# Kernel optimization log

Measured on AMD Instinct MI355X. Metric: run time of the kernel, lower is better.

Reference implementation:

```python
import jax, jax.numpy as jnp
import numpy as np

FEATURE_DIM = 16
NUM_HEADS = 16
HEAD_DIM = 64
R2 = float(np.sqrt(2.0))
RD = float(np.sqrt(FEATURE_DIM))        # sqrt(d) = 4
RRD = float(np.sqrt(RD))                # d^(1/4) = 2
RMS_EPS = 1e-5


def taylor_exp(x):
    # x: [b, h, l, d] -> [b, h, l, 1 + d + d*d]
    x2 = (x[..., :, None] * x[..., None, :]).reshape(*x.shape[:-1], FEATURE_DIM * FEATURE_DIM) / R2
    ones = jnp.ones_like(x[..., :1])
    return jnp.concatenate([ones, x / RRD, x2 / RD], axis=-1)


def setup_inputs() -> dict:
    key = jax.random.key(0)
    ks = jax.random.split(key, 5)
    b, l, d_model = 4, 2048, 1024
    inp = {
        'hidden_states': jax.random.normal(ks[0], (b, l, d_model), dtype=jnp.float32),
        'Wq': jax.random.normal(ks[1], (FEATURE_DIM * NUM_HEADS, d_model), dtype=jnp.float32) * 0.02,
        'Wk': jax.random.normal(ks[2], (FEATURE_DIM * NUM_HEADS, d_model), dtype=jnp.float32) * 0.02,
        'Wv': jax.random.normal(ks[3], (NUM_HEADS * HEAD_DIM, d_model), dtype=jnp.float32) * 0.02,
        'Wo': jax.random.normal(ks[4], (d_model, NUM_HEADS * HEAD_DIM), dtype=jnp.float32) * 0.02,
        'g_weight': jnp.ones((HEAD_DIM,), dtype=jnp.float32),
    }
    return inp


def reference(hidden_states, Wq, Wk, Wv, Wo, g_weight):
    b, l, _ = hidden_states.shape
    # projections (Linear, no bias): x @ W.T
    q = (hidden_states @ Wq.T).reshape(b, l, NUM_HEADS, FEATURE_DIM).transpose(0, 2, 1, 3)
    k = (hidden_states @ Wk.T).reshape(b, l, NUM_HEADS, FEATURE_DIM).transpose(0, 2, 1, 3)
    v = (hidden_states @ Wv.T).reshape(b, l, NUM_HEADS, HEAD_DIM).transpose(0, 2, 1, 3)

    qf = taylor_exp(q)  # [b, h, l, 273]
    kf = taylor_exp(k)  # [b, h, l, 273]

    A_qk = jnp.einsum('bhnd,bhmd->bhnm', qf, kf)
    A_qk = jnp.tril(A_qk)
    y = jnp.einsum('bhnm,bhme->bhne', A_qk, v)  # [b, h, l, head_dim]

    kv_state = jnp.einsum('bhnd,bhnf->bhfd', kf, v)[:, :, None]  # [b, h, 1, head_dim, 273]

    # RMSNorm over head_dim
    rms = jax.lax.rsqrt(jnp.mean(y * y, axis=-1, keepdims=True) + RMS_EPS)
    y = y * rms * g_weight

    y = y.transpose(0, 2, 1, 3).reshape(b, l, NUM_HEADS * HEAD_DIM)
    out = y @ Wo.T
    return out, kv_state
```

## Files before the change

kernel.cpp:

```cpp
#include <hip/hip_runtime.h>


typedef unsigned short u16;
typedef unsigned int u32;
typedef __attribute__((ext_vector_type(4))) float f32x4;
typedef __attribute__((ext_vector_type(16))) float f32x16;
typedef __attribute__((ext_vector_type(8))) short s16x8;

struct MaskT { static constexpr bool value = true;  };
struct MaskF { static constexpr bool value = false; };

__device__ __forceinline__ float bf2f(u16 u) {
    union { unsigned int i; float f; } x; x.i = ((unsigned int)u) << 16; return x.f;
}
__device__ __forceinline__ u16 f2bf(float f) {
    union { float f; unsigned int u; } x; x.f = f;
    unsigned int r = x.u + 0x7FFFu + ((x.u >> 16) & 1u);
    return (u16)(r >> 16);
}

typedef const __attribute__((address_space(1))) u32* gas1_t;
typedef __attribute__((address_space(3))) u32* las3_t;
__device__ __forceinline__ void gld16(const u16* g, u16* l) {
    __builtin_amdgcn_global_load_lds((gas1_t)(const void*)g, (las3_t)(void*)l, 16, 0, 0);
}

__global__ void detect_kernel(const unsigned int* __restrict__ H, int* __restrict__ flag)
{
    const int lane = threadIdx.x;
    int cnt = 0;
#pragma unroll
    for (int i = 0; i < 16; ++i) {
        const unsigned int wrd = H[lane * 16 + i];
        const int e = (int)((wrd >> 7) & 0xFFu);
        if (e >= 85 && e <= 170) ++cnt;
    }
    cnt += __shfl_xor(cnt, 1);  cnt += __shfl_xor(cnt, 2);
    cnt += __shfl_xor(cnt, 4);  cnt += __shfl_xor(cnt, 8);
    cnt += __shfl_xor(cnt, 16); cnt += __shfl_xor(cnt, 32);
    if (lane == 0) *flag = (cnt < 700) ? 1 : 0;
}

__global__ __launch_bounds__(256)
void cvt_all_kernel(const void* __restrict__ H,  const void* __restrict__ Wq,
                    const void* __restrict__ Wk, const void* __restrict__ Wv,
                    const void* __restrict__ Wo, const void* __restrict__ gw,
                    u16* __restrict__ Hb,  u16* __restrict__ Wqb,
                    u16* __restrict__ Wkb, u16* __restrict__ Wvb,
                    u16* __restrict__ Wob, u16* __restrict__ gwb,
                    const int* __restrict__ flag)
{
    const int f32in = *flag;
    const int NQ = 11010112 / 4;
    for (int qi = blockIdx.x * 256 + threadIdx.x; qi < NQ; qi += gridDim.x * 256) {
        const int i = qi * 4;
        const void* src; u16* dst; int off;
        if      (i <  8388608) { src = H;  dst = Hb;  off = i; }
        else if (i <  8650752) { src = Wq; dst = Wqb; off = i - 8388608; }
        else if (i <  8912896) { src = Wk; dst = Wkb; off = i - 8650752; }
        else if (i <  9961472) { src = Wv; dst = Wvb; off = i - 8912896; }
        else if (i < 11010048) { src = Wo; dst = Wob; off = i - 9961472; }
        else                   { src = gw; dst = gwb; off = i - 11010048; }
        ushort4 o;
        if (f32in) {
            const float4 v = *((const float4*)src + (off >> 2));
            o.x = f2bf(v.x); o.y = f2bf(v.y); o.z = f2bf(v.z); o.w = f2bf(v.w);
        } else {
            o = *((const ushort4*)src + (off >> 2));
        }
        *(ushort4*)(dst + off) = o;
    }
}

template<int MODE>
__global__ __launch_bounds__(256)
void gemm_nt(const u16* __restrict__ A,
             const u16* __restrict__ Bq, const u16* __restrict__ Bk,
             const u16* __restrict__ Bv,
             u16* __restrict__ Oq, u16* __restrict__ Ok,
             u16* __restrict__ Ovt, float* __restrict__ Of)
{
    __shared__ __attribute__((aligned(16))) u16 As[8192];
    __shared__ __attribute__((aligned(16))) u16 Bs[8192];
    const int t = threadIdx.x;
    const int lane = t & 63, w = t >> 6;
    const int c = lane & 15, qd = lane >> 4;
    const int wm = (w >> 1) * 64, wn = (w & 1) * 64;
    const int nwgx = gridDim.x;
    const int pid = blockIdx.y * nwgx + blockIdx.x;
    const int lid = (pid & 7) * ((nwgx * 64) >> 3) + (pid >> 3);
    const int rm = (lid / nwgx) * 128;
    const int cb = (lid % nwgx) * 128;

    const u16* Bsrc; int wrow0;
    if (MODE == 0) {
        if (cb < 256)      { Bsrc = Bq; wrow0 = cb; }
        else if (cb < 512) { Bsrc = Bk; wrow0 = cb - 256; }
        else               { Bsrc = Bv; wrow0 = cb - 512; }
    } else { Bsrc = Bq; wrow0 = cb; }

    f32x4 acc[4][4];
#pragma unroll
    for (int i = 0; i < 4; ++i)
#pragma unroll
        for (int j = 0; j < 4; ++j) acc[i][j] = (f32x4){0.f, 0.f, 0.f, 0.f};

    const int r0 = w * 8 + (lane >> 3);
    const int s0 = (lane & 7) ^ (lane >> 3);
    const u16* Ag = A    + (size_t)(rm    + r0) * 1024 + s0 * 8;
    const u16* Bg = Bsrc + (size_t)(wrow0 + r0) * 1024 + s0 * 8;
    u16* AsW = As + w * 512;
    u16* BsW = Bs + w * 512;

    for (int kt = 0; kt < 16; ++kt) {
        const int k0 = kt * 64;
        __syncthreads();
#pragma unroll
        for (int i = 0; i < 4; ++i) {
            gld16(Ag + (size_t)(i * 32) * 1024 + k0, AsW + i * 2048);
            gld16(Bg + (size_t)(i * 32) * 1024 + k0, BsW + i * 2048);
        }
        __syncthreads();
        s16x8 af[2][4], bfr[2][4];
#pragma unroll
        for (int kk = 0; kk < 2; ++kk) {
#pragma unroll
            for (int mt = 0; mt < 4; ++mt) {
                const int row = wm + mt * 16 + c;
                af[kk][mt] = *(const s16x8*)&As[row * 64 + (((kk * 4 + qd) ^ (row & 7)) * 8)];
            }
#pragma unroll
            for (int nt = 0; nt < 4; ++nt) {
                const int row = wn + nt * 16 + c;
                bfr[kk][nt] = *(const s16x8*)&Bs[row * 64 + (((kk * 4 + qd) ^ (row & 7)) * 8)];
            }
        }
#pragma unroll
        for (int kk = 0; kk < 2; ++kk)
#pragma unroll
            for (int mt = 0; mt < 4; ++mt)
#pragma unroll
                for (int nt = 0; nt < 4; ++nt)
                    acc[mt][nt] = __builtin_amdgcn_mfma_f32_16x16x32_bf16(af[kk][mt], bfr[kk][nt], acc[mt][nt], 0, 0, 0);
    }

#pragma unroll
    for (int mt = 0; mt < 4; ++mt) {
#pragma unroll
        for (int nt = 0; nt < 4; ++nt) {
            const int gc = cb + wn + nt * 16 + c;
            const int row0 = rm + wm + mt * 16 + qd * 4;
            if (MODE == 1) {
#pragma unroll
                for (int r = 0; r < 4; ++r)
                    Of[(size_t)(row0 + r) * 1024 + gc] = acc[mt][nt][r];
            } else if (gc < 512) {
#pragma unroll
                for (int r = 0; r < 4; ++r) {
                    const int row = row0 + r;
                    const int b_ = row >> 11, l_ = row & 2047;
                    const int cc = gc & 255;
                    const int h = cc >> 4, idx = cc & 15;
                    u16* dst = (gc < 256) ? Oq : Ok;
                    dst[(size_t)((b_ * 16 + h) * 2048 + l_) * 16 + idx] = f2bf(acc[mt][nt][r]);
                }
            } else {
                const int cc = gc - 512;
                const int h = cc >> 6, idx = cc & 63;
                const int b_ = row0 >> 11, l0 = row0 & 2047;
                ushort4 pk;
                pk.x = f2bf(acc[mt][nt][0]);
                pk.y = f2bf(acc[mt][nt][1]);
                pk.z = f2bf(acc[mt][nt][2]);
                pk.w = f2bf(acc[mt][nt][3]);
                *(ushort4*)(Ovt + ((size_t)((b_ * 16 + h) * 64 + idx)) * 2048 + l0) = pk;
            }
        }
    }
}

__global__ __launch_bounds__(512, 4)
void akv_kernel(const u16* __restrict__ Qg, const u16* __restrict__ Kg,
                const u16* __restrict__ Vt, const u16* __restrict__ gwb,
                u16* __restrict__ Yn, float* __restrict__ kvpart)
{
    __shared__ __attribute__((aligned(16))) char lds[61440];
    const int t = threadIdx.x, lane = t & 63, w = t >> 6;
    const int pid = blockIdx.y * 8 + blockIdx.x;
    const int x = pid & 7;
    const int cc = pid >> 3;

    if (cc < 32) {
        const int la = lane & 31, h = lane >> 5;
        const int bh = x * 8 + (cc >> 2);
        const int jj = cc & 3;
        const int b_ = bh >> 4, hh = bh & 15;
        const u16* Qh = Qg + (size_t)bh * (2048 * 16);
        const u16* Kh = Kg + (size_t)bh * (2048 * 16);
        const u16* Vh = Vt + (size_t)bh * (64 * 2048);
        const float gl0 = bf2f(gwb[la]);
        const float gl1 = bf2f(gwb[32 + la]);
        const f32x16 z16 = {0.f,0.f,0.f,0.f,0.f,0.f,0.f,0.f,
                            0.f,0.f,0.f,0.f,0.f,0.f,0.f,0.f};
        const int vbase0 = (la << 8) | (h << 4);
        const int vsw = (la & 7) << 4;
        u16* VsB = (u16*)lds;

        auto stageV = [&](int n0s, int bufsel) {
#pragma unroll
            for (int i = 0; i < 2; ++i) {
                const int slot = i * 512 + t;
                const int fl = slot >> 4;
                const int seg = (slot & 15) ^ (fl & 7);
                gld16(Vh + (size_t)fl * 2048 + n0s + seg * 8,
                      VsB + (size_t)bufsel * 8192 + (size_t)(i * 512 + (w << 6)) * 8);
            }
        };

        for (int pass = 0; pass < 2; ++pass) {
            const int qb = pass ? jj : (7 - jj);
            const int q0 = qb * 256 + w * 32;
            const int kf = 2 * qb + (w >> 2);
            const int wp = w & 3;
            const int nck = 2 * qb + 2;

            const s16x8 bq = *(const s16x8*)(Qh + (size_t)(q0 + la) * 16 + h * 8);
            f32x16 yt0 = z16, yt1 = z16;
            s16x8 ka[4];
            const char* vsc = (const char*)VsB;

            auto loadK = [&](s16x8* kk, int kcL) {
#pragma unroll
                for (int kt = 0; kt < 4; ++kt)
                    kk[kt] = *(const s16x8*)(Kh + (size_t)(kcL * 128 + kt * 32 + la) * 16 + h * 8);
            };

            auto tile = [&](int kt, auto MASKED) {
                constexpr bool masked = decltype(MASKED)::value;
                f32x16 sv = __builtin_amdgcn_mfma_f32_32x32x16_bf16(ka[kt], bq, z16, 0, 0, 0);
                float p[16];
#pragma unroll
                for (int r = 0; r < 16; ++r) {
                    const float s = sv[r];
                    float pv = fmaf(s, fmaf(s, 0.03125f, 0.25f), 1.0f);
                    if (masked) {
                        const int keyloc = (r & 3) + 8 * (r >> 2) + 4 * h;
                        if (keyloc > la) pv = 0.f;
                    }
                    p[r] = pv;
                }
#pragma unroll
                for (int ks = 0; ks < 2; ++ks) {
                    u32 X0, X1, Y0, Y1;
                    asm("v_cvt_pk_bf16_f32 %0, %1, %2" : "=v"(X0) : "v"(p[8*ks+0]), "v"(p[8*ks+1]));
                    asm("v_cvt_pk_bf16_f32 %0, %1, %2" : "=v"(X1) : "v"(p[8*ks+2]), "v"(p[8*ks+3]));
                    asm("v_cvt_pk_bf16_f32 %0, %1, %2" : "=v"(Y0) : "v"(p[8*ks+4]), "v"(p[8*ks+5]));
                    asm("v_cvt_pk_bf16_f32 %0, %1, %2" : "=v"(Y1) : "v"(p[8*ks+6]), "v"(p[8*ks+7]));
                    asm("v_permlane32_swap_b32 %0, %1" : "+v"(X0), "+v"(Y0));
                    asm("v_permlane32_swap_b32 %0, %1" : "+v"(X1), "+v"(Y1));
                    union { uint4 u; s16x8 v; } afu;
                    afu.u = (uint4){X0, X1, Y0, Y1};
                    const int offb = (kt << 6) | (ks << 5);
                    const s16x8 vb0 = *(const s16x8*)(vsc + (((vbase0 + offb)) ^ vsw));
                    const s16x8 vb1 = *(const s16x8*)(vsc + (((vbase0 + 8192 + offb)) ^ vsw));
                    yt0 = __builtin_amdgcn_mfma_f32_32x32x16_bf16(afu.v, vb0, yt0, 0, 0, 0);
                    yt1 = __builtin_amdgcn_mfma_f32_32x32x16_bf16(afu.v, vb1, yt1, 0, 0, 0);
                }
            };

            stageV(0, 0);
            loadK(ka, 0);
            __syncthreads();

            for (int kc = 0; kc < nck; ++kc) {
                const int cur = kc & 1;
                vsc = (const char*)(VsB + (size_t)cur * 8192);
                if (kc + 1 < nck) stageV((kc + 1) * 128, cur ^ 1);
                s16x8 kn[4] = {ka[0], ka[1], ka[2], ka[3]};
                if (kc < kf) loadK(kn, kc + 1);

                if (kc < kf) {
                    tile(0, MaskF{}); tile(1, MaskF{});
                    tile(2, MaskF{}); tile(3, MaskF{});
                } else if (kc == kf) {
                    if (wp == 0)      { tile(0, MaskT{}); }
                    else if (wp == 1) { tile(0, MaskF{}); tile(1, MaskT{}); }
                    else if (wp == 2) { tile(0, MaskF{}); tile(1, MaskF{}); tile(2, MaskT{}); }
                    else              { tile(0, MaskF{}); tile(1, MaskF{}); tile(2, MaskF{}); tile(3, MaskT{}); }
                }
                __syncthreads();
#pragma unroll
                for (int kt = 0; kt < 4; ++kt) ka[kt] = kn[kt];
            }

#pragma unroll
            for (int r = 0; r < 16; ++r) {
                float ss = yt0[r] * yt0[r] + yt1[r] * yt1[r];
                ss += __shfl_xor(ss, 1);  ss += __shfl_xor(ss, 2);
                ss += __shfl_xor(ss, 4);  ss += __shfl_xor(ss, 8);
                ss += __shfl_xor(ss, 16);
                const float rmsv = rsqrtf(ss * (1.0f / 64.0f) + 1e-5f);
                const int row = q0 + (r & 3) + 8 * (r >> 2) + 4 * h;
                u16* dst = Yn + ((size_t)(b_ * 2048 + row)) * 1024 + hh * 64;
                dst[la]      = f2bf(yt0[r] * rmsv * gl0);
                dst[32 + la] = f2bf(yt1[r] * rmsv * gl1);
            }
        }
    } else {
        const int c2 = cc - 32;
        const int bh = x * 8 + (c2 >> 2);
        const int ns = c2 & 3;
        const int c = lane & 15, qd = lane >> 4;
        const u16* Kh  = Kg + (size_t)bh * 2048 * 16;
        const u16* Vth = Vt + (size_t)bh * 64 * 2048;
        float (*kS)[20] = (float(*)[20])(lds);
        float (*kT)[20] = (float(*)[20])(lds + 5120);
        u16 (*KFs)[72]  = (u16(*)[72])(lds + 10240);
        u16 (*Vs)[72]   = (u16(*)[72])(lds + 51712);

        int i2a = 18, j2a = 18, i2b = 18, j2b = 18;
        if (t < 256) {
            const int dd = t;
            if (dd == 0)      { i2a = 16; j2a = 17; }
            else if (dd < 17) { i2a = dd - 1; j2a = 16; }
            else              { i2a = (dd - 17) >> 4; j2a = (dd - 17) & 15; }
            if (t < 32) {
                const int d2 = 256 + t;
                if (d2 < 273) { i2b = (d2 - 17) >> 4; j2b = (d2 - 17) & 15; }
            }
        }

        f32x4 acc[4][5];
#pragma unroll
        for (int mt = 0; mt < 4; ++mt)
#pragma unroll
            for (int j = 0; j < 5; ++j) acc[mt][j] = (f32x4){0.f, 0.f, 0.f, 0.f};

        for (int ch = 0; ch < 8; ++ch) {
            const int n0 = ns * 512 + ch * 64;
            __syncthreads();
            if (t < 128) {
                const int row = t >> 1, half = t & 1;
                uint4 kv = *(const uint4*)(Kh + (size_t)(n0 + row) * 16 + half * 8);
                const u16* ke = (const u16*)&kv;
#pragma unroll
                for (int e = 0; e < 8; ++e) {
                    const float f = bf2f(ke[e]);
                    kS[row][half * 8 + e] = f;
                    kT[row][half * 8 + e] = f * 0.17677669529663687f;
                }
            } else if (t < 192) {
                const int row = t - 128;
                kS[row][16] = 1.f;  kS[row][17] = 1.f;  kS[row][18] = 0.f;
                kT[row][16] = 0.5f; kT[row][17] = 1.f;  kT[row][18] = 0.f;
            }
            if (t < 256) {
#pragma unroll
                for (int i = 0; i < 2; ++i) {
                    const int lin = i * 256 + t;
                    const int f = lin >> 3, seg = lin & 7;
                    *(uint4*)&Vs[f][seg * 8] =
                        *(const uint4*)(Vth + (size_t)f * 2048 + n0 + seg * 8);
                }
            }
            __syncthreads();
            if (t < 256) {
                unsigned int* dst = (unsigned int*)&KFs[t][0];
#pragma unroll 8
                for (int i = 0; i < 32; ++i) {
                    const float v0 = kS[2 * i][i2a]     * kT[2 * i][j2a];
                    const float v1 = kS[2 * i + 1][i2a] * kT[2 * i + 1][j2a];
                    dst[i] = (unsigned int)f2bf(v0) | ((unsigned int)f2bf(v1) << 16);
                }
                if (t < 32) {
                    unsigned int* dst2 = (unsigned int*)&KFs[256 + t][0];
#pragma unroll 8
                    for (int i = 0; i < 32; ++i) {
                        const float v0 = kS[2 * i][i2b]     * kT[2 * i][j2b];
                        const float v1 = kS[2 * i + 1][i2b] * kT[2 * i + 1][j2b];
                        dst2[i] = (unsigned int)f2bf(v0) | ((unsigned int)f2bf(v1) << 16);
                    }
                }
            }
            __syncthreads();
            if (t < 256) {
#pragma unroll
                for (int kt = 0; kt < 2; ++kt) {
                    s16x8 va[4];
#pragma unroll
                    for (int mt = 0; mt < 4; ++mt)
                        va[mt] = *(const s16x8*)&Vs[mt * 16 + c][kt * 32 + qd * 8];
#pragma unroll
                    for (int j = 0; j < 5; ++j) {
                        const int dt = w + 4 * j;
                        if (dt < 18) {
                            s16x8 vb = *(const s16x8*)&KFs[dt * 16 + c][kt * 32 + qd * 8];
#pragma unroll
                            for (int mt = 0; mt < 4; ++mt)
                                acc[mt][j] = __builtin_amdgcn_mfma_f32_16x16x32_bf16(va[mt], vb, acc[mt][j], 0, 0, 0);
                        }
                    }
                }
            }
        }

        if (t < 256) {
            float* base = kvpart + ((size_t)(ns * 64 + bh) * 64) * 273;
#pragma unroll
            for (int j = 0; j < 5; ++j) {
                const int dt = w + 4 * j;
                if (dt >= 18) continue;
                const int dd = dt * 16 + c;
                if (dd >= 273) continue;
#pragma unroll
                for (int mt = 0; mt < 4; ++mt)
#pragma unroll
                    for (int r = 0; r < 4; ++r) {
                        const int f = mt * 16 + qd * 4 + r;
                        base[f * 273 + dd] = acc[mt][j][r];
                    }
            }
        }
    }
}

__global__ __launch_bounds__(256)
void kv_fin_kernel(const float* __restrict__ kvpart, float* __restrict__ o)
{
    const int i = blockIdx.x * 256 + threadIdx.x;
    const int S = 64 * 64 * 273;
    if (i < S)
        o[i] = kvpart[i] + kvpart[i + S] + kvpart[i + 2 * S] + kvpart[i + 3 * S];
}

extern "C" void kernel_launch(void* const* d_in, const int* in_sizes, int n_in,
                              void* d_out, int out_size, void* d_ws, size_t ws_size,
                              hipStream_t stream)
{
    const void* H  = d_in[0];
    const void* Wq = d_in[1];
    const void* Wk = d_in[2];
    const void* Wv = d_in[3];
    const void* Wo = d_in[4];
    const void* gw = d_in[5];
    float* outf = (float*)d_out;

    char* ws = (char*)d_ws;
    const size_t M = 1 << 20;
    u16*   Hb    = (u16*)(ws);
    u16*   Wqb   = (u16*)(ws + 16 * M);
    u16*   Wkb   = (u16*)(ws + 16 * M + 512 * 1024);
    u16*   Wvb   = (u16*)(ws + 17 * M);
    u16*   Wob   = (u16*)(ws + 19 * M);
    u16*   gwb   = (u16*)(ws + 21 * M);
    int*   flag  = (int*)(ws + 21 * M + 4096);
    u16*   q     = (u16*)(ws + 22 * M);
    u16*   k     = (u16*)(ws + 26 * M);
    u16*   vt    = (u16*)(ws + 30 * M);
    float* kvpart= (float*)(ws + 46 * M);
    u16*   yn    = Hb;

    detect_kernel<<<1, 64, 0, stream>>>((const unsigned int*)H, flag);
    cvt_all_kernel<<<2048, 256, 0, stream>>>(H, Wq, Wk, Wv, Wo, gw,
                                             Hb, Wqb, Wkb, Wvb, Wob, gwb, flag);

    gemm_nt<0><<<dim3(12, 64), 256, 0, stream>>>(Hb, Wqb, Wkb, Wvb, q, k, vt, nullptr);
    akv_kernel<<<dim3(8, 64), 512, 0, stream>>>(q, k, vt, gwb, yn, kvpart);
    kv_fin_kernel<<<4368, 256, 0, stream>>>(kvpart, outf + (size_t)8388608);
    gemm_nt<1><<<dim3(8, 64), 256, 0, stream>>>(yn, Wob, nullptr, nullptr,
                                                nullptr, nullptr, nullptr, outf);
}
```

Baseline: 228.0 us.

## Split fused attention/kv kernel into separate attention and kv-state kernels

The fused kernel, which mixed causal-attention blocks and kv-state blocks in one grid, becomes two launches. The attention kernel now gives each block a single query chunk instead of two paired chunks, which doubles the block count but drops the pairing that balanced causal work across blocks. The kv-state accumulation moves to its own 256-thread kernel, so the 256 idle threads per block in the old kv path go away. The cost is an extra launch, the two workloads no longer running concurrently, and uneven per-block work in attention.

```diff
diff --git a/kernel.cpp b/kernel.cpp
--- a/kernel.cpp
+++ b/kernel.cpp
@@ -180,247 +180,240 @@
 }
 
 __global__ __launch_bounds__(512, 4)
-void akv_kernel(const u16* __restrict__ Qg, const u16* __restrict__ Kg,
-                const u16* __restrict__ Vt, const u16* __restrict__ gwb,
-                u16* __restrict__ Yn, float* __restrict__ kvpart)
-{
-    __shared__ __attribute__((aligned(16))) char lds[61440];
+void attn_kernel(const u16* __restrict__ Qg, const u16* __restrict__ Kg,
+                 const u16* __restrict__ Vt, const u16* __restrict__ gwb,
+                 u16* __restrict__ Yn)
+{
+    __shared__ __attribute__((aligned(16))) u16 Vs[2][8192];
     const int t = threadIdx.x, lane = t & 63, w = t >> 6;
+    const int la = lane & 31, h = lane >> 5;
     const int pid = blockIdx.y * 8 + blockIdx.x;
     const int x = pid & 7;
-    const int cc = pid >> 3;
-
-    if (cc < 32) {
-        const int la = lane & 31, h = lane >> 5;
-        const int bh = x * 8 + (cc >> 2);
-        const int jj = cc & 3;
-        const int b_ = bh >> 4, hh = bh & 15;
-        const u16* Qh = Qg + (size_t)bh * (2048 * 16);
-        const u16* Kh = Kg + (size_t)bh * (2048 * 16);
-        const u16* Vh = Vt + (size_t)bh * (64 * 2048);
-        const float gl0 = bf2f(gwb[la]);
-        const float gl1 = bf2f(gwb[32 + la]);
-        const f32x16 z16 = {0.f,0.f,0.f,0.f,0.f,0.f,0.f,0.f,
-                            0.f,0.f,0.f,0.f,0.f,0.f,0.f,0.f};
-        const int vbase0 = (la << 8) | (h << 4);
-        const int vsw = (la & 7) << 4;
-        u16* VsB = (u16*)lds;
-
-        auto stageV = [&](int n0s, int bufsel) {
-#pragma unroll
-            for (int i = 0; i < 2; ++i) {
-                const int slot = i * 512 + t;
-                const int fl = slot >> 4;
-                const int seg = (slot & 15) ^ (fl & 7);
-                gld16(Vh + (size_t)fl * 2048 + n0s + seg * 8,
-                      VsB + (size_t)bufsel * 8192 + (size_t)(i * 512 + (w << 6)) * 8);
-            }
-        };
-
-        for (int pass = 0; pass < 2; ++pass) {
-            const int qb = pass ? jj : (7 - jj);
-            const int q0 = qb * 256 + w * 32;
-            const int kf = 2 * qb + (w >> 2);
-            const int wp = w & 3;
-            const int nck = 2 * qb + 2;
-
-            const s16x8 bq = *(const s16x8*)(Qh + (size_t)(q0 + la) * 16 + h * 8);
-            f32x16 yt0 = z16, yt1 = z16;
-            s16x8 ka[4];
-            const char* vsc = (const char*)VsB;
-
-            auto loadK = [&](s16x8* kk, int kcL) {
-#pragma unroll
-                for (int kt = 0; kt < 4; ++kt)
-                    kk[kt] = *(const s16x8*)(Kh + (size_t)(kcL * 128 + kt * 32 + la) * 16 + h * 8);
-            };
-
-            auto tile = [&](int kt, auto MASKED) {
-                constexpr bool masked = decltype(MASKED)::value;
-                f32x16 sv = __builtin_amdgcn_mfma_f32_32x32x16_bf16(ka[kt], bq, z16, 0, 0, 0);
-                float p[16];
-#pragma unroll
-                for (int r = 0; r < 16; ++r) {
-                    const float s = sv[r];
-                    float pv = fmaf(s, fmaf(s, 0.03125f, 0.25f), 1.0f);
-                    if (masked) {
-                        const int keyloc = (r & 3) + 8 * (r >> 2) + 4 * h;
-                        if (keyloc > la) pv = 0.f;
-                    }
-                    p[r] = pv;
-                }
-#pragma unroll
-                for (int ks = 0; ks < 2; ++ks) {
-                    u32 X0, X1, Y0, Y1;
-                    asm("v_cvt_pk_bf16_f32 %0, %1, %2" : "=v"(X0) : "v"(p[8*ks+0]), "v"(p[8*ks+1]));
-                    asm("v_cvt_pk_bf16_f32 %0, %1, %2" : "=v"(X1) : "v"(p[8*ks+2]), "v"(p[8*ks+3]));
-                    asm("v_cvt_pk_bf16_f32 %0, %1, %2" : "=v"(Y0) : "v"(p[8*ks+4]), "v"(p[8*ks+5]));
-                    asm("v_cvt_pk_bf16_f32 %0, %1, %2" : "=v"(Y1) : "v"(p[8*ks+6]), "v"(p[8*ks+7]));
-                    asm("v_permlane32_swap_b32 %0, %1" : "+v"(X0), "+v"(Y0));
-                    asm("v_permlane32_swap_b32 %0, %1" : "+v"(X1), "+v"(Y1));
-                    union { uint4 u; s16x8 v; } afu;
-                    afu.u = (uint4){X0, X1, Y0, Y1};
-                    const int offb = (kt << 6) | (ks << 5);
-                    const s16x8 vb0 = *(const s16x8*)(vsc + (((vbase0 + offb)) ^ vsw));
-                    const s16x8 vb1 = *(const s16x8*)(vsc + (((vbase0 + 8192 + offb)) ^ vsw));
-                    yt0 = __builtin_amdgcn_mfma_f32_32x32x16_bf16(afu.v, vb0, yt0, 0, 0, 0);
-                    yt1 = __builtin_amdgcn_mfma_f32_32x32x16_bf16(afu.v, vb1, yt1, 0, 0, 0);
-                }
-            };
-
-            stageV(0, 0);
-            loadK(ka, 0);
-            __syncthreads();
-
-            for (int kc = 0; kc < nck; ++kc) {
-                const int cur = kc & 1;
-                vsc = (const char*)(VsB + (size_t)cur * 8192);
-                if (kc + 1 < nck) stageV((kc + 1) * 128, cur ^ 1);
-                s16x8 kn[4] = {ka[0], ka[1], ka[2], ka[3]};
-                if (kc < kf) loadK(kn, kc + 1);
-
-                if (kc < kf) {
-                    tile(0, MaskF{}); tile(1, MaskF{});
-                    tile(2, MaskF{}); tile(3, MaskF{});
-                } else if (kc == kf) {
-                    if (wp == 0)      { tile(0, MaskT{}); }
-                    else if (wp == 1) { tile(0, MaskF{}); tile(1, MaskT{}); }
-                    else if (wp == 2) { tile(0, MaskF{}); tile(1, MaskF{}); tile(2, MaskT{}); }
-                    else              { tile(0, MaskF{}); tile(1, MaskF{}); tile(2, MaskF{}); tile(3, MaskT{}); }
-                }
-                __syncthreads();
-#pragma unroll
-                for (int kt = 0; kt < 4; ++kt) ka[kt] = kn[kt];
-            }
-
-#pragma unroll
-            for (int r = 0; r < 16; ++r) {
-                float ss = yt0[r] * yt0[r] + yt1[r] * yt1[r];
-                ss += __shfl_xor(ss, 1);  ss += __shfl_xor(ss, 2);
-                ss += __shfl_xor(ss, 4);  ss += __shfl_xor(ss, 8);
-                ss += __shfl_xor(ss, 16);
-                const float rmsv = rsqrtf(ss * (1.0f / 64.0f) + 1e-5f);
-                const int row = q0 + (r & 3) + 8 * (r >> 2) + 4 * h;
-                u16* dst = Yn + ((size_t)(b_ * 2048 + row)) * 1024 + hh * 64;
-                dst[la]      = f2bf(yt0[r] * rmsv * gl0);
-                dst[32 + la] = f2bf(yt1[r] * rmsv * gl1);
-            }
-        }
-    } else {
-        const int c2 = cc - 32;
-        const int bh = x * 8 + (c2 >> 2);
-        const int ns = c2 & 3;
-        const int c = lane & 15, qd = lane >> 4;
-        const u16* Kh  = Kg + (size_t)bh * 2048 * 16;
-        const u16* Vth = Vt + (size_t)bh * 64 * 2048;
-        float (*kS)[20] = (float(*)[20])(lds);
-        float (*kT)[20] = (float(*)[20])(lds + 5120);
-        u16 (*KFs)[72]  = (u16(*)[72])(lds + 10240);
-        u16 (*Vs)[72]   = (u16(*)[72])(lds + 51712);
-
-        int i2a = 18, j2a = 18, i2b = 18, j2b = 18;
-        if (t < 256) {
-            const int dd = t;
-            if (dd == 0)      { i2a = 16; j2a = 17; }
-            else if (dd < 17) { i2a = dd - 1; j2a = 16; }
-            else              { i2a = (dd - 17) >> 4; j2a = (dd - 17) & 15; }
+    const int yy = pid >> 3;
+    const int bh = x * 8 + (yy >> 3);
+    const int jj = yy & 3;
+    const int pass = (yy >> 2) & 1;
+    const int qb = pass ? jj : (7 - jj);
+    const int b_ = bh >> 4, hh = bh & 15;
+    const u16* Qh = Qg + (size_t)bh * (2048 * 16);
+    const u16* Kh = Kg + (size_t)bh * (2048 * 16);
+    const u16* Vh = Vt + (size_t)bh * (64 * 2048);
+    const float gl0 = bf2f(gwb[la]);
+    const float gl1 = bf2f(gwb[32 + la]);
+    const f32x16 z16 = {0.f,0.f,0.f,0.f,0.f,0.f,0.f,0.f,
+                        0.f,0.f,0.f,0.f,0.f,0.f,0.f,0.f};
+    const int vbase0 = (la << 8) | (h << 4);
+    const int vsw = (la & 7) << 4;
+
+    auto stageV = [&](int n0s, int bufsel) {
+#pragma unroll
+        for (int i = 0; i < 2; ++i) {
+            const int slot = i * 512 + t;
+            const int fl = slot >> 4;
+            const int seg = (slot & 15) ^ (fl & 7);
+            gld16(Vh + (size_t)fl * 2048 + n0s + seg * 8,
+                  (u16*)Vs[bufsel] + (size_t)(i * 512 + (w << 6)) * 8);
+        }
+    };
+
+    const int q0 = qb * 256 + w * 32;
+    const int kf = 2 * qb + (w >> 2);
+    const int wp = w & 3;
+    const int nck = 2 * qb + 2;
+
+    const s16x8 bq = *(const s16x8*)(Qh + (size_t)(q0 + la) * 16 + h * 8);
+    f32x16 yt0 = z16, yt1 = z16;
+    s16x8 ka[4];
+    const char* vsc = (const char*)Vs[0];
+
+    auto loadK = [&](s16x8* kk, int kcL) {
+#pragma unroll
+        for (int kt = 0; kt < 4; ++kt)
+            kk[kt] = *(const s16x8*)(Kh + (size_t)(kcL * 128 + kt * 32 + la) * 16 + h * 8);
+    };
+
+    auto tile = [&](int kt, auto MASKED) {
+        constexpr bool masked = decltype(MASKED)::value;
+        f32x16 sv = __builtin_amdgcn_mfma_f32_32x32x16_bf16(ka[kt], bq, z16, 0, 0, 0);
+        float p[16];
+#pragma unroll
+        for (int r = 0; r < 16; ++r) {
+            const float s = sv[r];
+            float pv = fmaf(s, fmaf(s, 0.03125f, 0.25f), 1.0f);
+            if (masked) {
+                const int keyloc = (r & 3) + 8 * (r >> 2) + 4 * h;
+                if (keyloc > la) pv = 0.f;
+            }
+            p[r] = pv;
+        }
+#pragma unroll
+        for (int ks = 0; ks < 2; ++ks) {
+            u32 X0, X1, Y0, Y1;
+            asm("v_cvt_pk_bf16_f32 %0, %1, %2" : "=v"(X0) : "v"(p[8*ks+0]), "v"(p[8*ks+1]));
+            asm("v_cvt_pk_bf16_f32 %0, %1, %2" : "=v"(X1) : "v"(p[8*ks+2]), "v"(p[8*ks+3]));
+            asm("v_cvt_pk_bf16_f32 %0, %1, %2" : "=v"(Y0) : "v"(p[8*ks+4]), "v"(p[8*ks+5]));
+            asm("v_cvt_pk_bf16_f32 %0, %1, %2" : "=v"(Y1) : "v"(p[8*ks+6]), "v"(p[8*ks+7]));
+            asm("v_permlane32_swap_b32 %0, %1" : "+v"(X0), "+v"(Y0));
+            asm("v_permlane32_swap_b32 %0, %1" : "+v"(X1), "+v"(Y1));
+            union { uint4 u; s16x8 v; } afu;
+            afu.u = (uint4){X0, X1, Y0, Y1};
+            const int offb = (kt << 6) | (ks << 5);
+            const s16x8 vb0 = *(const s16x8*)(vsc + (((vbase0 + offb)) ^ vsw));
+            const s16x8 vb1 = *(const s16x8*)(vsc + (((vbase0 + 8192 + offb)) ^ vsw));
+            yt0 = __builtin_amdgcn_mfma_f32_32x32x16_bf16(afu.v, vb0, yt0, 0, 0, 0);
+            yt1 = __builtin_amdgcn_mfma_f32_32x32x16_bf16(afu.v, vb1, yt1, 0, 0, 0);
+        }
+    };
+
+    stageV(0, 0);
+    loadK(ka, 0);
+    __syncthreads();
+
+    for (int kc = 0; kc < nck; ++kc) {
+        const int cur = kc & 1;
+        vsc = (const char*)Vs[cur];
+        if (kc + 1 < nck) stageV((kc + 1) * 128, cur ^ 1);
+        s16x8 kn[4] = {ka[0], ka[1], ka[2], ka[3]};
+        if (kc < kf) loadK(kn, kc + 1);
+
+        if (kc < kf) {
+            tile(0, MaskF{}); tile(1, MaskF{});
+            tile(2, MaskF{}); tile(3, MaskF{});
+        } else if (kc == kf) {
+            if (wp == 0)      { tile(0, MaskT{}); }
+            else if (wp == 1) { tile(0, MaskF{}); tile(1, MaskT{}); }
+            else if (wp == 2) { tile(0, MaskF{}); tile(1, MaskF{}); tile(2, MaskT{}); }
+            else              { tile(0, MaskF{}); tile(1, MaskF{}); tile(2, MaskF{}); tile(3, MaskT{}); }
+        }
+        __syncthreads();
+#pragma unroll
+        for (int kt = 0; kt < 4; ++kt) ka[kt] = kn[kt];
+    }
+
+#pragma unroll
+    for (int r = 0; r < 16; ++r) {
+        float ss = yt0[r] * yt0[r] + yt1[r] * yt1[r];
+        ss += __shfl_xor(ss, 1);  ss += __shfl_xor(ss, 2);
+        ss += __shfl_xor(ss, 4);  ss += __shfl_xor(ss, 8);
+        ss += __shfl_xor(ss, 16);
+        const float rmsv = rsqrtf(ss * (1.0f / 64.0f) + 1e-5f);
+        const int row = q0 + (r & 3) + 8 * (r >> 2) + 4 * h;
+        u16* dst = Yn + ((size_t)(b_ * 2048 + row)) * 1024 + hh * 64;
+        dst[la]      = f2bf(yt0[r] * rmsv * gl0);
+        dst[32 + la] = f2bf(yt1[r] * rmsv * gl1);
+    }
+}
+
+__global__ __launch_bounds__(256)
+void kv_mfma_kernel(const u16* __restrict__ Kg, const u16* __restrict__ Vt,
+                    float* __restrict__ kvpart)
+{
+    __shared__ __attribute__((aligned(16))) float kS[64][20];
+    __shared__ __attribute__((aligned(16))) float kT[64][20];
+    __shared__ __attribute__((aligned(16))) u16 KFs[288][72];
+    __shared__ __attribute__((aligned(16))) u16 Vs[64][72];
+    const int t = threadIdx.x, lane = t & 63, w = t >> 6;
+    const int c = lane & 15, qd = lane >> 4;
+    const int ns = blockIdx.x, bh = blockIdx.y;
+    const u16* Kh  = Kg + (size_t)bh * 2048 * 16;
+    const u16* Vth = Vt + (size_t)bh * 64 * 2048;
+
+    int i2a, j2a, i2b = 18, j2b = 18;
+    {
+        const int dd = t;
+        if (dd == 0)      { i2a = 16; j2a = 17; }
+        else if (dd < 17) { i2a = dd - 1; j2a = 16; }
+        else              { i2a = (dd - 17) >> 4; j2a = (dd - 17) & 15; }
+        if (t < 32) {
+            const int d2 = 256 + t;
+            if (d2 < 273) { i2b = (d2 - 17) >> 4; j2b = (d2 - 17) & 15; }
+        }
+    }
+
+    f32x4 acc[4][5];
+#pragma unroll
+    for (int mt = 0; mt < 4; ++mt)
+#pragma unroll
+        for (int j = 0; j < 5; ++j) acc[mt][j] = (f32x4){0.f, 0.f, 0.f, 0.f};
+
+    for (int ch = 0; ch < 8; ++ch) {
+        const int n0 = ns * 512 + ch * 64;
+        __syncthreads();
+        if (t < 128) {
+            const int row = t >> 1, half = t & 1;
+            uint4 kv = *(const uint4*)(Kh + (size_t)(n0 + row) * 16 + half * 8);
+            const u16* ke = (const u16*)&kv;
+#pragma unroll
+            for (int e = 0; e < 8; ++e) {
+                const float f = bf2f(ke[e]);
+                kS[row][half * 8 + e] = f;
+                kT[row][half * 8 + e] = f * 0.17677669529663687f;
+            }
+        } else if (t < 192) {
+            const int row = t - 128;
+            kS[row][16] = 1.f;  kS[row][17] = 1.f;  kS[row][18] = 0.f;
+            kT[row][16] = 0.5f; kT[row][17] = 1.f;  kT[row][18] = 0.f;
+        }
+#pragma unroll
+        for (int i = 0; i < 2; ++i) {
+            const int lin = i * 256 + t;
+            const int f = lin >> 3, seg = lin & 7;
+            *(uint4*)&Vs[f][seg * 8] =
+                *(const uint4*)(Vth + (size_t)f * 2048 + n0 + seg * 8);
+        }
+        __syncthreads();
+        {
+            unsigned int* dst = (unsigned int*)&KFs[t][0];
+#pragma unroll 8
+            for (int i = 0; i < 32; ++i) {
+                const float v0 = kS[2 * i][i2a]     * kT[2 * i][j2a];
+                const float v1 = kS[2 * i + 1][i2a] * kT[2 * i + 1][j2a];
+                dst[i] = (unsigned int)f2bf(v0) | ((unsigned int)f2bf(v1) << 16);
+            }
             if (t < 32) {
-                const int d2 = 256 + t;
-                if (d2 < 273) { i2b = (d2 - 17) >> 4; j2b = (d2 - 17) & 15; }
-            }
-        }
-
-        f32x4 acc[4][5];
-#pragma unroll
-        for (int mt = 0; mt < 4; ++mt)
-#pragma unroll
-            for (int j = 0; j < 5; ++j) acc[mt][j] = (f32x4){0.f, 0.f, 0.f, 0.f};
-
-        for (int ch = 0; ch < 8; ++ch) {
-            const int n0 = ns * 512 + ch * 64;
-            __syncthreads();
-            if (t < 128) {
-                const int row = t >> 1, half = t & 1;
-                uint4 kv = *(const uint4*)(Kh + (size_t)(n0 + row) * 16 + half * 8);
-                const u16* ke = (const u16*)&kv;
-#pragma unroll
-                for (int e = 0; e < 8; ++e) {
-                    const float f = bf2f(ke[e]);
-                    kS[row][half * 8 + e] = f;
-                    kT[row][half * 8 + e] = f * 0.17677669529663687f;
-                }
-            } else if (t < 192) {
-                const int row = t - 128;
-                kS[row][16] = 1.f;  kS[row][17] = 1.f;  kS[row][18] = 0.f;
-                kT[row][16] = 0.5f; kT[row][17] = 1.f;  kT[row][18] = 0.f;
-            }
-            if (t < 256) {
-#pragma unroll
-                for (int i = 0; i < 2; ++i) {
-                    const int lin = i * 256 + t;
-                    const int f = lin >> 3, seg = lin & 7;
-                    *(uint4*)&Vs[f][seg * 8] =
-                        *(const uint4*)(Vth + (size_t)f * 2048 + n0 + seg * 8);
-                }
-            }
-            __syncthreads();
-            if (t < 256) {
-                unsigned int* dst = (unsigned int*)&KFs[t][0];
+                unsigned int* dst2 = (unsigned int*)&KFs[256 + t][0];
 #pragma unroll 8
                 for (int i = 0; i < 32; ++i) {
-                    const float v0 = kS[2 * i][i2a]     * kT[2 * i][j2a];
-                    const float v1 = kS[2 * i + 1][i2a] * kT[2 * i + 1][j2a];
-                    dst[i] = (unsigned int)f2bf(v0) | ((unsigned int)f2bf(v1) << 16);
+                    const float v0 = kS[2 * i][i2b]     * kT[2 * i][j2b];
+                    const float v1 = kS[2 * i + 1][i2b] * kT[2 * i + 1][j2b];
+                    dst2[i] = (unsigned int)f2bf(v0) | ((unsigned int)f2bf(v1) << 16);
                 }
-                if (t < 32) {
-                    unsigned int* dst2 = (unsigned int*)&KFs[256 + t][0];
-#pragma unroll 8
-                    for (int i = 0; i < 32; ++i) {
-                        const float v0 = kS[2 * i][i2b]     * kT[2 * i][j2b];
-                        const float v1 = kS[2 * i + 1][i2b] * kT[2 * i + 1][j2b];
-                        dst2[i] = (unsigned int)f2bf(v0) | ((unsigned int)f2bf(v1) << 16);
-                    }
-                }
-            }
-            __syncthreads();
-            if (t < 256) {
-#pragma unroll
-                for (int kt = 0; kt < 2; ++kt) {
-                    s16x8 va[4];
-#pragma unroll
-                    for (int mt = 0; mt < 4; ++mt)
-                        va[mt] = *(const s16x8*)&Vs[mt * 16 + c][kt * 32 + qd * 8];
-#pragma unroll
-                    for (int j = 0; j < 5; ++j) {
-                        const int dt = w + 4 * j;
-                        if (dt < 18) {
-                            s16x8 vb = *(const s16x8*)&KFs[dt * 16 + c][kt * 32 + qd * 8];
-#pragma unroll
-                            for (int mt = 0; mt < 4; ++mt)
-                                acc[mt][j] = __builtin_amdgcn_mfma_f32_16x16x32_bf16(va[mt], vb, acc[mt][j], 0, 0, 0);
-                        }
-                    }
-                }
-            }
-        }
-
-        if (t < 256) {
-            float* base = kvpart + ((size_t)(ns * 64 + bh) * 64) * 273;
+            }
+        }
+        __syncthreads();
+#pragma unroll
+        for (int kt = 0; kt < 2; ++kt) {
+            s16x8 va[4];
+#pragma unroll
+            for (int mt = 0; mt < 4; ++mt)
+                va[mt] = *(const s16x8*)&Vs[mt * 16 + c][kt * 32 + qd * 8];
 #pragma unroll
             for (int j = 0; j < 5; ++j) {
                 const int dt = w + 4 * j;
-                if (dt >= 18) continue;
-                const int dd = dt * 16 + c;
-                if (dd >= 273) continue;
-#pragma unroll
-                for (int mt = 0; mt < 4; ++mt)
-#pragma unroll
-                    for (int r = 0; r < 4; ++r) {
-                        const int f = mt * 16 + qd * 4 + r;
-                        base[f * 273 + dd] = acc[mt][j][r];
-                    }
-            }
-        }
+                if (dt < 18) {
+                    s16x8 vb = *(const s16x8*)&KFs[dt * 16 + c][kt * 32 + qd * 8];
+#pragma unroll
+                    for (int mt = 0; mt < 4; ++mt)
+                        acc[mt][j] = __builtin_amdgcn_mfma_f32_16x16x32_bf16(va[mt], vb, acc[mt][j], 0, 0, 0);
+                }
+            }
+        }
+    }
+
+    float* base = kvpart + ((size_t)(ns * 64 + bh) * 64) * 273;
+#pragma unroll
+    for (int j = 0; j < 5; ++j) {
+        const int dt = w + 4 * j;
+        if (dt >= 18) continue;
+        const int dd = dt * 16 + c;
+        if (dd >= 273) continue;
+#pragma unroll
+        for (int mt = 0; mt < 4; ++mt)
+#pragma unroll
+            for (int r = 0; r < 4; ++r) {
+                const int f = mt * 16 + qd * 4 + r;
+                base[f * 273 + dd] = acc[mt][j][r];
+            }
     }
 }
 
@@ -465,7 +458,8 @@
                                              Hb, Wqb, Wkb, Wvb, Wob, gwb, flag);
 
     gemm_nt<0><<<dim3(12, 64), 256, 0, stream>>>(Hb, Wqb, Wkb, Wvb, q, k, vt, nullptr);
-    akv_kernel<<<dim3(8, 64), 512, 0, stream>>>(q, k, vt, gwb, yn, kvpart);
+    attn_kernel<<<dim3(8, 64), 512, 0, stream>>>(q, k, vt, gwb, yn);
+    kv_mfma_kernel<<<dim3(4, 64), 256, 0, stream>>>(k, vt, kvpart);
     kv_fin_kernel<<<4368, 256, 0, stream>>>(kvpart, outf + (size_t)8388608);
     gemm_nt<1><<<dim3(8, 64), 256, 0, stream>>>(yn, Wob, nullptr, nullptr,
                                                 nullptr, nullptr, nullptr, outf);
```

After: 241.1 us. +5.8%, slower.
